# Optimization experiments

Hardware: AMD Instinct MI355X
Metric: run time of the kernel (lower is better)

The kernel has to match this reference:

```python
import jax, jax.numpy as jnp
import numpy as np

B, S1, S2, D1, D2 = 4, 2048, 2048, 512, 512
H, DK, DV = 8, 64, 64


def setup_inputs() -> dict:
    key = jax.random.key(0)
    ks = jax.random.split(key, 8)
    x1 = jax.random.normal(ks[0], (B, S1, D1), dtype=jnp.float32)
    x2 = jax.random.normal(ks[1], (B, S2, D2), dtype=jnp.float32)
    x3 = jax.random.normal(ks[2], (B, S2, D2), dtype=jnp.float32)
    s = 0.02
    Wq = jax.random.normal(ks[3], (D1, H * DK), dtype=jnp.float32) * s
    Wk = jax.random.normal(ks[4], (D2, H * DK), dtype=jnp.float32) * s
    Wv = jax.random.normal(ks[5], (D2, H * DV), dtype=jnp.float32) * s
    Wo = jax.random.normal(ks[6], (H * DV, D1), dtype=jnp.float32) * s
    bo = jnp.zeros((D1,), dtype=jnp.float32)
    return {"x1": x1, "x2": x2, "x3": x3, "Wq": Wq, "Wk": Wk, "Wv": Wv, "Wo": Wo, "bo": bo}


def reference(x1, x2, x3, Wq, Wk, Wv, Wo, bo):
    b, s1, _ = x1.shape
    # project to per-head q, k, v: [B, H, S, Dh]
    q = (x1 @ Wq).reshape(b, s1, H, DK).transpose(0, 2, 1, 3)
    k = (x2 @ Wk).reshape(b, x2.shape[1], H, DK).transpose(0, 2, 1, 3)
    v = (x3 @ Wv).reshape(b, x3.shape[1], H, DV).transpose(0, 2, 1, 3)
    scores = jnp.einsum('bhqd,bhkd->bhqk', q, k) / jnp.sqrt(jnp.float32(DK))
    attn = jax.nn.softmax(scores, axis=-1)
    out = jnp.einsum('bhqk,bhkd->bhqd', attn, v)  # [B, H, S1, DV]
    out = out.transpose(0, 2, 1, 3).reshape(b, s1, H * DV)
    return out @ Wo + bo
```

## Files before the change

kernel.cpp:

```cpp
#include <hip/hip_runtime.h>

typedef __attribute__((ext_vector_type(4))) float f32x4;
typedef __attribute__((ext_vector_type(8))) __bf16 bf16x8;
typedef __attribute__((ext_vector_type(4))) __bf16 bf16x4;

#define DEVINL __device__ __forceinline__

DEVINL void gld16(const void* g, void* l) {
  __builtin_amdgcn_global_load_lds((__attribute__((address_space(1))) void*)(void*)g,
                                   (__attribute__((address_space(3))) void*)l, 16, 0, 0);
}


__global__ __launch_bounds__(256) void cvt_all(const float* x1, const float* x2, const float* x3,
                                               const float* Wq, const float* Wk, const float* Wv,
                                               const float* Wo, __bf16* o0, __bf16* o1, __bf16* o2,
                                               __bf16* WT) {
  __shared__ float t[64][65];
  const int bx = blockIdx.x;
  if (bx < 12288) {
    const int z = bx >> 12;
    const float* s = z == 0 ? x1 : z == 1 ? x2 : x3;
    __bf16* d = z == 0 ? o0 : z == 1 ? o1 : o2;
    size_t i = (size_t)(bx & 4095) * 256 + threadIdx.x;
    f32x4 v = ((const f32x4*)s)[i];
    bf16x4 o;
#pragma unroll
    for (int j = 0; j < 4; ++j) o[j] = (__bf16)v[j];
    ((bf16x4*)d)[i] = o;
  } else {
    const int l = bx - 12288;
    const int z = l >> 6;
    const float* W = z == 0 ? Wq : z == 1 ? Wk : z == 2 ? Wv : Wo;
    __bf16* D = WT + (size_t)z * 512 * 512;
    const int r0 = ((l >> 3) & 7) * 64, c0 = (l & 7) * 64;
    const int tx = threadIdx.x & 63, ty = threadIdx.x >> 6;
#pragma unroll
    for (int j = 0; j < 16; ++j)
      t[ty + j * 4][tx] = W[(size_t)(r0 + ty + j * 4) * 512 + c0 + tx];
    __syncthreads();
#pragma unroll
    for (int j = 0; j < 16; ++j)
      D[(size_t)(c0 + ty + j * 4) * 512 + r0 + tx] = (__bf16)t[tx][ty + j * 4];
  }
}


DEVINL void gemm_tile(const __bf16* A, const __bf16* Bt, int m0, int n0,
                      __bf16* As, __bf16* Bs, f32x4 acc[4][4]) {
  const int tid = threadIdx.x, lane = tid & 63, w = tid >> 6;
  const int qd = lane >> 4, r = lane & 15;
  const int wm = w & 1, wn = w >> 1;
  const char* ap[4];
  const char* bp[4];
#pragma unroll
  for (int j = 0; j < 4; ++j) {
    int c = (w * 4 + j) * 64 + lane;
    int row = c >> 3, cs = c & 7;
    int gc = cs ^ (row & 7);
    ap[j] = (const char*)A + (size_t)(m0 + row) * 1024 + gc * 16;
    bp[j] = (const char*)Bt + (size_t)(n0 + row) * 1024 + gc * 16;
  }
  int offA[4][2], offB[4][2];
#pragma unroll
  for (int t = 0; t < 4; ++t)
#pragma unroll
    for (int ks = 0; ks < 2; ++ks) {
      int m = wm * 64 + t * 16 + r;
      offA[t][ks] = m * 128 + (((ks * 4 + qd) ^ (m & 7)) * 16);
      int n = wn * 64 + t * 16 + r;
      offB[t][ks] = n * 128 + (((ks * 4 + qd) ^ (n & 7)) * 16);
    }
  char* AsC = (char*)As;
  char* BsC = (char*)Bs;
  for (int kt = 0; kt < 8; ++kt) {
    __syncthreads();
#pragma unroll
    for (int j = 0; j < 4; ++j) {
      gld16(ap[j] + kt * 128, AsC + (w * 4 + j) * 1024);
      gld16(bp[j] + kt * 128, BsC + (w * 4 + j) * 1024);
    }
    __syncthreads();
#pragma unroll
    for (int ks = 0; ks < 2; ++ks) {
      bf16x8 a[4], b[4];
#pragma unroll
      for (int t = 0; t < 4; ++t) {
        a[t] = *(const bf16x8*)(AsC + offA[t][ks]);
        b[t] = *(const bf16x8*)(BsC + offB[t][ks]);
      }
#pragma unroll
      for (int i = 0; i < 4; ++i)
#pragma unroll
        for (int j2 = 0; j2 < 4; ++j2)
          acc[i][j2] = __builtin_amdgcn_mfma_f32_16x16x32_bf16(a[i], b[j2], acc[i][j2], 0, 0, 0);
    }
  }
}

__global__ __launch_bounds__(256, 3) void gemm_proj(const __bf16* x1b, const __bf16* x2b,
                                                    const __bf16* x3b, const __bf16* WT,
                                                    __bf16* Qo, __bf16* Ko, __bf16* Vto) {
  __shared__ __align__(16) char smem[34816];
  __bf16* As = (__bf16*)smem;
  __bf16* Bs = (__bf16*)(smem + 16384);
  const int z = blockIdx.z;
  const __bf16* A = z == 0 ? x1b : z == 1 ? x2b : x3b;
  const __bf16* Bt = WT + (size_t)z * 512 * 512;
  const int l = blockIdx.x;
  const int sidx = l >> 3;
  const int m0 = ((l & 7) * 8 + (sidx >> 2)) * 128;
  const int n0 = (sidx & 3) * 128;
  f32x4 acc[4][4] = {};
  gemm_tile(A, Bt, m0, n0, As, Bs, acc);
  const int tid = threadIdx.x, lane = tid & 63, w = tid >> 6;
  const int qd = lane >> 4, r = lane & 15, wm = w & 1, wn = w >> 1;
  const int b = m0 >> 11, sbase = m0 & 2047;
  if (z == 2) {
    __syncthreads();
    char* T = smem;
#pragma unroll
    for (int mt = 0; mt < 4; ++mt)
#pragma unroll
      for (int nt = 0; nt < 4; ++nt) {
        int dv = wn * 64 + nt * 16 + r;
        int sl = wm * 64 + mt * 16 + qd * 4;
        bf16x4 p4;
#pragma unroll
        for (int g = 0; g < 4; ++g) p4[g] = (__bf16)acc[mt][nt][g];
        *(bf16x4*)(T + (size_t)dv * 272 + sl * 2) = p4;
      }
    __syncthreads();
#pragma unroll
    for (int p2 = 0; p2 < 2; ++p2) {
      int dvrow = p2 * 64 + (tid >> 2);
      int col = n0 + dvrow, h = col >> 6, d = col & 63;
      __bf16* dst = Vto + ((size_t)(b * 8 + h) * 64 + d) * 2048 + sbase + (tid & 3) * 8;
#pragma unroll
      for (int j = 0; j < 4; ++j) {
        bf16x8 vv = *(const bf16x8*)(T + (size_t)dvrow * 272 + (tid & 3) * 16 + j * 64);
        *(bf16x8*)(dst + j * 32) = vv;
      }
    }
  } else {
    const float qscale = 0.18033688f;
#pragma unroll
    for (int mt = 0; mt < 4; ++mt) {
#pragma unroll
      for (int nt = 0; nt < 4; ++nt) {
        f32x4 v = acc[mt][nt];
        if (z == 0) {
#pragma unroll
          for (int g = 0; g < 4; ++g) v[g] *= qscale;
        }
        int col = n0 + wn * 64 + nt * 16 + r;
        int h = col >> 6, d = col & 63;
        int s = sbase + wm * 64 + mt * 16 + qd * 4;
        __bf16* O = (z == 0 ? Qo : Ko) + ((size_t)(b * 8 + h) * 2048 + s) * 64 + d;
#pragma unroll
        for (int g = 0; g < 4; ++g) O[(size_t)g * 64] = (__bf16)v[g];
      }
    }
  }
}

__global__ __launch_bounds__(256, 2) void gemm_out(const __bf16* Ob, const __bf16* WoT,
                                                   const float* bo, float* out) {
  __shared__ __align__(16) __bf16 As[64 * 64];
  __shared__ __align__(16) __bf16 Bs[128 * 64];
  const int tid = threadIdx.x, lane = tid & 63, w = tid >> 6;
  const int qd = lane >> 4, r = lane & 15, wm = w & 1, wn = w >> 1;
  const int id = blockIdx.x;
  const int rest = id >> 3;
  const int m0 = ((id & 7) * 16 + (rest & 15)) * 64;
  const int n0 = (rest >> 4) * 128;
  const char* ap[2];
  const char* bp[4];
#pragma unroll
  for (int j = 0; j < 2; ++j) {
    int c = (w * 2 + j) * 64 + lane;
    int row = c >> 3, gc = (c & 7) ^ (row & 7);
    ap[j] = (const char*)Ob + (size_t)(m0 + row) * 1024 + gc * 16;
  }
#pragma unroll
  for (int j = 0; j < 4; ++j) {
    int c = (w * 4 + j) * 64 + lane;
    int row = c >> 3, gc = (c & 7) ^ (row & 7);
    bp[j] = (const char*)WoT + (size_t)(n0 + row) * 1024 + gc * 16;
  }
  int offA[2][2], offB[4][2];
#pragma unroll
  for (int ks = 0; ks < 2; ++ks) {
#pragma unroll
    for (int t = 0; t < 2; ++t) {
      int m = wm * 32 + t * 16 + r;
      offA[t][ks] = m * 128 + (((ks * 4 + qd) ^ (m & 7)) * 16);
    }
#pragma unroll
    for (int t = 0; t < 4; ++t) {
      int n = wn * 64 + t * 16 + r;
      offB[t][ks] = n * 128 + (((ks * 4 + qd) ^ (n & 7)) * 16);
    }
  }
  char* AsC = (char*)As;
  char* BsC = (char*)Bs;
  f32x4 acc[2][4] = {};
  for (int kt = 0; kt < 8; ++kt) {
    __syncthreads();
#pragma unroll
    for (int j = 0; j < 2; ++j) gld16(ap[j] + kt * 128, AsC + (w * 2 + j) * 1024);
#pragma unroll
    for (int j = 0; j < 4; ++j) gld16(bp[j] + kt * 128, BsC + (w * 4 + j) * 1024);
    __syncthreads();
#pragma unroll
    for (int ks = 0; ks < 2; ++ks) {
      bf16x8 a[2], b[4];
#pragma unroll
      for (int t = 0; t < 2; ++t) a[t] = *(const bf16x8*)(AsC + offA[t][ks]);
#pragma unroll
      for (int t = 0; t < 4; ++t) b[t] = *(const bf16x8*)(BsC + offB[t][ks]);
#pragma unroll
      for (int i = 0; i < 2; ++i)
#pragma unroll
        for (int j2 = 0; j2 < 4; ++j2)
          acc[i][j2] = __builtin_amdgcn_mfma_f32_16x16x32_bf16(a[i], b[j2], acc[i][j2], 0, 0, 0);
    }
  }
#pragma unroll
  for (int nt = 0; nt < 4; ++nt) {
    int col = n0 + wn * 64 + nt * 16 + r;
    float bv = bo[col];
#pragma unroll
    for (int mt = 0; mt < 2; ++mt) {
      int mg = m0 + wm * 32 + mt * 16 + qd * 4;
#pragma unroll
      for (int g = 0; g < 4; ++g) out[(size_t)(mg + g) * 512 + col] = acc[mt][nt][g] + bv;
    }
  }
}

__global__ __launch_bounds__(256, 4) void attn(const __bf16* Q, const __bf16* K,
                                               const __bf16* Vt, __bf16* Opart, float* Lp) {
  __shared__ __align__(16) __bf16 QPs[128 * 64];
  __shared__ __align__(16) __bf16 Ksd[2][64 * 64];
  __shared__ __align__(16) __bf16 Vs[64 * 64];
  const int tid = threadIdx.x, lane = tid & 63, w = tid >> 6;
  const int qd = lane >> 4, r = lane & 15;
  const int id = blockIdx.x;
  const int rest = id >> 3;
  const int bh = (id & 7) * 4 + (rest >> 5);
  const int kvh = (rest >> 4) & 1;
  const int q0 = (rest & 15) * 128;
  const __bf16* Qg = Q + ((size_t)bh * 2048 + q0) * 64;
  const __bf16* Kg = K + (size_t)bh * 2048 * 64;
  const __bf16* Vg = Vt + (size_t)bh * 64 * 2048;
  char* PsC = (char*)QPs;
  char* Ks0 = (char*)Ksd;
  char* Ks1 = (char*)Ksd + 8192;
  char* VsC = (char*)Vs;

  const char* Kst[2];
  const char* Vst[2];
  int ldso[2];
#pragma unroll
  for (int j = 0; j < 2; ++j) {
    int c = (w * 2 + j) * 64 + lane;
    int m = c >> 3, gc = (c & 7) ^ (m & 7);
    Kst[j] = (const char*)Kg + (size_t)m * 128 + gc * 16;
    Vst[j] = (const char*)Vg + (size_t)m * 4096 + gc * 16;
    ldso[j] = (w * 2 + j) * 1024;
  }

  const int kt0 = kvh * 16;

#pragma unroll
  for (int j = 0; j < 4; ++j) {
    int c = (w * 4 + j) * 64 + lane;
    int m = c >> 3, gc = (c & 7) ^ (m & 7);
    gld16((const char*)Qg + m * 128 + gc * 16, PsC + (w * 4 + j) * 1024);
  }
#pragma unroll
  for (int j = 0; j < 2; ++j) gld16(Kst[j] + (size_t)kt0 * 8192, Ks0 + ldso[j]);
  __syncthreads();

  bf16x8 qf[2][2];
#pragma unroll
  for (int mt = 0; mt < 2; ++mt)
#pragma unroll
    for (int ks = 0; ks < 2; ++ks) {
      int m = w * 32 + mt * 16 + r;
      qf[mt][ks] = *(const bf16x8*)(PsC + m * 128 + ((ks * 4 + qd) ^ (m & 7)) * 16);
    }

  int offKV[4][2];
#pragma unroll
  for (int t = 0; t < 4; ++t)
#pragma unroll
    for (int ks = 0; ks < 2; ++ks) {
      int n = t * 16 + r;
      offKV[t][ks] = n * 128 + ((ks * 4 + qd) ^ (n & 7)) * 16;
    }

  bf16x8 ones;
#pragma unroll
  for (int j = 0; j < 8; ++j) ones[j] = (__bf16)1.0f;
  const f32x4 z4 = {};

  f32x4 oacc[2][4] = {};
  f32x4 lacc[2] = {};

  auto iter = [&](int kt, int ktn, char* Kc, char* Kn) {
    __syncthreads();
#pragma unroll
    for (int j = 0; j < 2; ++j) {
      gld16(Vst[j] + (size_t)kt * 128, VsC + ldso[j]);
      gld16(Kst[j] + (size_t)ktn * 8192, Kn + ldso[j]);
    }

    f32x4 sf[2][4];
#pragma unroll
    for (int nt = 0; nt < 4; ++nt) {
      bf16x8 kf0 = *(const bf16x8*)(Kc + offKV[nt][0]);
      bf16x8 kf1 = *(const bf16x8*)(Kc + offKV[nt][1]);
#pragma unroll
      for (int mt = 0; mt < 2; ++mt) {
        f32x4 t0 = __builtin_amdgcn_mfma_f32_16x16x32_bf16(kf0, qf[mt][0], z4, 0, 0, 0);
        sf[mt][nt] = __builtin_amdgcn_mfma_f32_16x16x32_bf16(kf1, qf[mt][1], t0, 0, 0, 0);
      }
    }
#pragma unroll
    for (int mt = 0; mt < 2; ++mt) {
      int q = w * 32 + mt * 16 + r;
#pragma unroll
      for (int nt = 0; nt < 4; ++nt) {
        bf16x4 p4;
#pragma unroll
        for (int g = 0; g < 4; ++g) p4[g] = (__bf16)__builtin_exp2f(sf[mt][nt][g]);
        *(bf16x4*)(PsC + q * 128 + (((2 * nt + (qd >> 1)) ^ (q & 7)) * 16) + (qd & 1) * 8) = p4;
      }
    }

    __syncthreads();

#pragma unroll
    for (int mt = 0; mt < 2; ++mt) {
      int q = w * 32 + mt * 16 + r;
      bf16x8 pf0 = *(const bf16x8*)(PsC + q * 128 + ((qd ^ (q & 7)) * 16));
      bf16x8 pf1 = *(const bf16x8*)(PsC + q * 128 + (((4 + qd) ^ (q & 7)) * 16));
      lacc[mt] = __builtin_amdgcn_mfma_f32_16x16x32_bf16(pf0, ones, lacc[mt], 0, 0, 0);
      lacc[mt] = __builtin_amdgcn_mfma_f32_16x16x32_bf16(pf1, ones, lacc[mt], 0, 0, 0);
#pragma unroll
      for (int dvt = 0; dvt < 4; ++dvt) {
        bf16x8 vf0 = *(const bf16x8*)(VsC + offKV[dvt][0]);
        bf16x8 vf1 = *(const bf16x8*)(VsC + offKV[dvt][1]);
        oacc[mt][dvt] = __builtin_amdgcn_mfma_f32_16x16x32_bf16(pf0, vf0, oacc[mt][dvt], 0, 0, 0);
        oacc[mt][dvt] = __builtin_amdgcn_mfma_f32_16x16x32_bf16(pf1, vf1, oacc[mt][dvt], 0, 0, 0);
      }
    }
  };

#pragma unroll 1
  for (int kt = kt0; kt < kt0 + 16; kt += 2) {
    iter(kt, kt + 1, Ks0, Ks1);
    int kt2 = (kt + 2 < kt0 + 16) ? kt + 2 : kt + 1;
    iter(kt + 1, kt2, Ks1, Ks0);
  }

  const size_t pbase = (size_t)(kvh * 32 + bh) * 2048;
#pragma unroll
  for (int mt = 0; mt < 2; ++mt) {
    if (r == 0) {
#pragma unroll
      for (int g = 0; g < 4; ++g)
        Lp[pbase + q0 + w * 32 + mt * 16 + qd * 4 + g] = lacc[mt][g];
    }
  }
  __bf16* Ob0 = Opart + pbase * 64;
#pragma unroll
  for (int mt = 0; mt < 2; ++mt) {
#pragma unroll
    for (int g = 0; g < 4; ++g) {
      int s = q0 + w * 32 + mt * 16 + qd * 4 + g;
#pragma unroll
      for (int dvt = 0; dvt < 4; ++dvt)
        Ob0[(size_t)s * 64 + dvt * 16 + r] = (__bf16)oacc[mt][dvt][g];
    }
  }
}

__global__ __launch_bounds__(256) void combine(const __bf16* Op, const float* Lp, __bf16* Ob) {
  int c = blockIdx.x * 256 + threadIdx.x;
  int bhs = c >> 3;
  int dv0 = (c & 7) * 8;
  size_t e = (size_t)bhs * 64 + dv0;
  bf16x8 a = *(const bf16x8*)(Op + e);
  bf16x8 b2 = *(const bf16x8*)(Op + ((size_t)32 * 2048 * 64) + e);
  float inv = 1.0f / (Lp[bhs] + Lp[bhs + 65536]);
  int bh = bhs >> 11, s = bhs & 2047, b = bh >> 3, h = bh & 7;
  bf16x8 o;
#pragma unroll
  for (int j = 0; j < 8; ++j) o[j] = (__bf16)(((float)a[j] + (float)b2[j]) * inv);
  *(bf16x8*)(Ob + ((size_t)(b * 2048 + s)) * 512 + h * 64 + dv0) = o;
}


extern "C" void kernel_launch(void* const* d_in, const int* in_sizes, int n_in,
                              void* d_out, int out_size, void* d_ws, size_t ws_size,
                              hipStream_t stream) {
  const float* x1 = (const float*)d_in[0];
  const float* x2 = (const float*)d_in[1];
  const float* x3 = (const float*)d_in[2];
  const float* Wq = (const float*)d_in[3];
  const float* Wk = (const float*)d_in[4];
  const float* Wv = (const float*)d_in[5];
  const float* Wo = (const float*)d_in[6];
  const float* bo = (const float*)d_in[7];
  float* out = (float*)d_out;
  char* ws = (char*)d_ws;
  const size_t MB = 1ull << 20;
  __bf16* x1b = (__bf16*)(ws);
  __bf16* x2b = (__bf16*)(ws + 8 * MB);
  __bf16* x3b = (__bf16*)(ws + 16 * MB);
  __bf16* WT = (__bf16*)(ws + 24 * MB);
  __bf16* Qb = (__bf16*)(ws + 26 * MB);
  __bf16* Kb = (__bf16*)(ws + 34 * MB);
  __bf16* Vtb = (__bf16*)(ws + 42 * MB);
  __bf16* Ob = (__bf16*)(ws + 50 * MB);
  __bf16* Opart = (__bf16*)(ws + 58 * MB);
  float* Lp = (float*)(ws + 74 * MB);

  cvt_all<<<dim3(12544), 256, 0, stream>>>(x1, x2, x3, Wq, Wk, Wv, Wo, x1b, x2b, x3b, WT);
  gemm_proj<<<dim3(256, 1, 3), 256, 0, stream>>>(x1b, x2b, x3b, WT, Qb, Kb, Vtb);
  attn<<<dim3(1024), 256, 0, stream>>>(Qb, Kb, Vtb, Opart, Lp);
  combine<<<dim3(2048), 256, 0, stream>>>(Opart, Lp, Ob);
  gemm_out<<<dim3(512), 256, 0, stream>>>(Ob, WT + 3ull * 512 * 512, bo, out);
}
```

Measured before the change: 189.9 us.

## Fuse split-KV combine into output GEMM and pipeline attention barriers

Removes the separate combine kernel. The output projection GEMM now loads both partial attention outputs and the two partial softmax denominators, merges and normalizes them in registers, and writes the A tile into LDS itself, with the next head prefetched ahead of the compute. Separately, the attention loop swaps __syncthreads for explicit vmcnt waits plus raw s_barrier, and raises wave priority around the MFMA sections so K/V loads overlap compute. This saves one launch and a round trip of the combined output through global memory. In exchange, the GEMM's A loads become register-staged rather than async, and the hand-written waitcnt accounting must stay correct.

After: 191.1 us. Within noise of the previous version (+0.6%).

```diff
diff --git a/kernel.cpp b/kernel.cpp
--- a/kernel.cpp
+++ b/kernel.cpp
@@ -164,8 +164,9 @@
   }
 }
 
-__global__ __launch_bounds__(256, 2) void gemm_out(const __bf16* Ob, const __bf16* WoT,
-                                                   const float* bo, float* out) {
+__global__ __launch_bounds__(256, 2) void gemm_out(const __bf16* Op, const float* Lp,
+                                                   const __bf16* WoT, const float* bo,
+                                                   float* out) {
   __shared__ __align__(16) __bf16 As[64 * 64];
   __shared__ __align__(16) __bf16 Bs[128 * 64];
   const int tid = threadIdx.x, lane = tid & 63, w = tid >> 6;
@@ -174,20 +175,22 @@
   const int rest = id >> 3;
   const int m0 = ((id & 7) * 16 + (rest & 15)) * 64;
   const int n0 = (rest >> 4) * 128;
-  const char* ap[2];
+  const int b8 = (m0 >> 11) * 8;
+  const int sb = m0 & 2047;
   const char* bp[4];
-#pragma unroll
-  for (int j = 0; j < 2; ++j) {
-    int c = (w * 2 + j) * 64 + lane;
-    int row = c >> 3, gc = (c & 7) ^ (row & 7);
-    ap[j] = (const char*)Ob + (size_t)(m0 + row) * 1024 + gc * 16;
-  }
 #pragma unroll
   for (int j = 0; j < 4; ++j) {
     int c = (w * 4 + j) * 64 + lane;
     int row = c >> 3, gc = (c & 7) ^ (row & 7);
     bp[j] = (const char*)WoT + (size_t)(n0 + row) * 1024 + gc * 16;
   }
+  int arow[2], ach[2];
+#pragma unroll
+  for (int j = 0; j < 2; ++j) {
+    int c = (w * 2 + j) * 64 + lane;
+    arow[j] = c >> 3;
+    ach[j] = c & 7;
+  }
   int offA[2][2], offB[4][2];
 #pragma unroll
   for (int ks = 0; ks < 2; ++ks) {
@@ -204,14 +207,34 @@
   }
   char* AsC = (char*)As;
   char* BsC = (char*)Bs;
+  bf16x8 pa0[2], pa1[2];
+  float pinv[2];
+  auto loadA = [&](int h) {
+#pragma unroll
+    for (int j = 0; j < 2; ++j) {
+      size_t rr = (size_t)(b8 + h) * 2048 + sb + arow[j];
+      const __bf16* p0 = Op + rr * 64 + ach[j] * 8;
+      pa0[j] = *(const bf16x8*)p0;
+      pa1[j] = *(const bf16x8*)(p0 + (size_t)32 * 2048 * 64);
+      pinv[j] = 1.0f / (Lp[rr] + Lp[rr + 65536]);
+    }
+  };
+  loadA(0);
   f32x4 acc[2][4] = {};
   for (int kt = 0; kt < 8; ++kt) {
     __syncthreads();
 #pragma unroll
-    for (int j = 0; j < 2; ++j) gld16(ap[j] + kt * 128, AsC + (w * 2 + j) * 1024);
-#pragma unroll
     for (int j = 0; j < 4; ++j) gld16(bp[j] + kt * 128, BsC + (w * 4 + j) * 1024);
-    __syncthreads();
+#pragma unroll
+    for (int j = 0; j < 2; ++j) {
+      bf16x8 q;
+#pragma unroll
+      for (int k2 = 0; k2 < 8; ++k2)
+        q[k2] = (__bf16)(((float)pa0[j][k2] + (float)pa1[j][k2]) * pinv[j]);
+      *(bf16x8*)(AsC + arow[j] * 128 + (ach[j] ^ (arow[j] & 7)) * 16) = q;
+    }
+    __syncthreads();
+    if (kt < 7) loadA(kt + 1);
 #pragma unroll
     for (int ks = 0; ks < 2; ++ks) {
       bf16x8 a[2], b[4];
@@ -281,7 +304,10 @@
   }
 #pragma unroll
   for (int j = 0; j < 2; ++j) gld16(Kst[j] + (size_t)kt0 * 8192, Ks0 + ldso[j]);
-  __syncthreads();
+  asm volatile("s_waitcnt vmcnt(0)" ::: "memory");
+  __builtin_amdgcn_sched_barrier(0);
+  __builtin_amdgcn_s_barrier();
+  __builtin_amdgcn_sched_barrier(0);
 
   bf16x8 qf[2][2];
 #pragma unroll
@@ -310,14 +336,14 @@
   f32x4 lacc[2] = {};
 
   auto iter = [&](int kt, int ktn, char* Kc, char* Kn) {
-    __syncthreads();
-#pragma unroll
-    for (int j = 0; j < 2; ++j) {
-      gld16(Vst[j] + (size_t)kt * 128, VsC + ldso[j]);
-      gld16(Kst[j] + (size_t)ktn * 8192, Kn + ldso[j]);
-    }
+    gld16(Vst[0] + (size_t)kt * 128, VsC + ldso[0]);
+    gld16(Vst[1] + (size_t)kt * 128, VsC + ldso[1]);
+    gld16(Kst[0] + (size_t)ktn * 8192, Kn + ldso[0]);
+    gld16(Kst[1] + (size_t)ktn * 8192, Kn + ldso[1]);
+    __builtin_amdgcn_sched_barrier(0);
 
     f32x4 sf[2][4];
+    __builtin_amdgcn_s_setprio(1);
 #pragma unroll
     for (int nt = 0; nt < 4; ++nt) {
       bf16x8 kf0 = *(const bf16x8*)(Kc + offKV[nt][0]);
@@ -328,6 +354,7 @@
         sf[mt][nt] = __builtin_amdgcn_mfma_f32_16x16x32_bf16(kf1, qf[mt][1], t0, 0, 0, 0);
       }
     }
+    __builtin_amdgcn_s_setprio(0);
 #pragma unroll
     for (int mt = 0; mt < 2; ++mt) {
       int q = w * 32 + mt * 16 + r;
@@ -340,8 +367,12 @@
       }
     }
 
-    __syncthreads();
-
+    asm volatile("s_waitcnt vmcnt(2)" ::: "memory");
+    __builtin_amdgcn_sched_barrier(0);
+    __builtin_amdgcn_s_barrier();
+    __builtin_amdgcn_sched_barrier(0);
+
+    __builtin_amdgcn_s_setprio(1);
 #pragma unroll
     for (int mt = 0; mt < 2; ++mt) {
       int q = w * 32 + mt * 16 + r;
@@ -357,6 +388,12 @@
         oacc[mt][dvt] = __builtin_amdgcn_mfma_f32_16x16x32_bf16(pf1, vf1, oacc[mt][dvt], 0, 0, 0);
       }
     }
+    __builtin_amdgcn_s_setprio(0);
+
+    asm volatile("s_waitcnt vmcnt(0)" ::: "memory");
+    __builtin_amdgcn_sched_barrier(0);
+    __builtin_amdgcn_s_barrier();
+    __builtin_amdgcn_sched_barrier(0);
   };
 
 #pragma unroll 1
@@ -386,21 +423,6 @@
         Ob0[(size_t)s * 64 + dvt * 16 + r] = (__bf16)oacc[mt][dvt][g];
     }
   }
-}
-
-__global__ __launch_bounds__(256) void combine(const __bf16* Op, const float* Lp, __bf16* Ob) {
-  int c = blockIdx.x * 256 + threadIdx.x;
-  int bhs = c >> 3;
-  int dv0 = (c & 7) * 8;
-  size_t e = (size_t)bhs * 64 + dv0;
-  bf16x8 a = *(const bf16x8*)(Op + e);
-  bf16x8 b2 = *(const bf16x8*)(Op + ((size_t)32 * 2048 * 64) + e);
-  float inv = 1.0f / (Lp[bhs] + Lp[bhs + 65536]);
-  int bh = bhs >> 11, s = bhs & 2047, b = bh >> 3, h = bh & 7;
-  bf16x8 o;
-#pragma unroll
-  for (int j = 0; j < 8; ++j) o[j] = (__bf16)(((float)a[j] + (float)b2[j]) * inv);
-  *(bf16x8*)(Ob + ((size_t)(b * 2048 + s)) * 512 + h * 64 + dv0) = o;
 }
 
 
@@ -425,13 +447,11 @@
   __bf16* Qb = (__bf16*)(ws + 26 * MB);
   __bf16* Kb = (__bf16*)(ws + 34 * MB);
   __bf16* Vtb = (__bf16*)(ws + 42 * MB);
-  __bf16* Ob = (__bf16*)(ws + 50 * MB);
   __bf16* Opart = (__bf16*)(ws + 58 * MB);
   float* Lp = (float*)(ws + 74 * MB);
 
   cvt_all<<<dim3(12544), 256, 0, stream>>>(x1, x2, x3, Wq, Wk, Wv, Wo, x1b, x2b, x3b, WT);
   gemm_proj<<<dim3(256, 1, 3), 256, 0, stream>>>(x1b, x2b, x3b, WT, Qb, Kb, Vtb);
   attn<<<dim3(1024), 256, 0, stream>>>(Qb, Kb, Vtb, Opart, Lp);
-  combine<<<dim3(2048), 256, 0, stream>>>(Opart, Lp, Ob);
-  gemm_out<<<dim3(512), 256, 0, stream>>>(Ob, WT + 3ull * 512 * 512, bo, out);
-}
+  gemm_out<<<dim3(512), 256, 0, stream>>>(Opart, Lp, WT + 3ull * 512 * 512, bo, out);
+}
```
